# Kernel tuning notes

Measured on AMD Instinct MI355X. Metric: run time of the kernel, lower is better.

Reference implementation:

```python
import jax, jax.numpy as jnp
import numpy as np

B, D = 32768, 512
DEPTH = 7
ORDERS = (1, 2, 3, 5)
COUPLING_STRENGTH = 1.0


def _damping_coeffs():
    # frequency_dependent profile: 0.1 / (1 + exp(linspace(0, 3, D)))
    freqs = jnp.exp(jnp.linspace(0.0, 3.0, D))
    return 0.1 / (1.0 + freqs)


def _generate_harmonics(wave, hmats):
    acc = jnp.zeros_like(wave)
    for order, H in zip(ORDERS, hmats):
        hw = wave @ H.astype(wave.dtype)
        if order == 1:
            h = hw
        elif order == 2:
            h = hw * jnp.conj(hw)
        elif order == 3:
            h = hw * jnp.conj(hw) * hw
        else:
            mag = jnp.abs(hw)
            ph = jnp.angle(hw)
            h = (mag ** (1.0 / order)) * jnp.exp(1j * (ph * float(order)))
        acc = acc + h * (1.0 / (order * order))
    return acc


def _nonlinearity(wave, scale, bias):
    re = jnp.tanh(wave.real * scale + bias)
    im = jnp.tanh(wave.imag * scale + bias)
    return jax.lax.complex(re, im)


def _forward(wave_real, wave_imag, coupling_matrix, harmonic_1, harmonic_2,
             harmonic_3, harmonic_5, mixing_scale, mixing_bias):
    wave = jax.lax.complex(wave_real, wave_imag)  # [B, D] complex64
    hmats = (harmonic_1, harmonic_2, harmonic_3, harmonic_5)
    damping = _damping_coeffs()  # [D], non-trainable constant

    chamber = wave
    history = []
    for depth in range(DEPTH):
        transformed = (chamber @ coupling_matrix.astype(chamber.dtype)) * COUPLING_STRENGTH
        with_harmonics = transformed + _generate_harmonics(chamber, hmats)
        if depth > 0:
            # InterferenceLayer approximated as complex wave superposition
            interference = chamber + with_harmonics
        else:
            interference = with_harmonics
        nl = _nonlinearity(interference, mixing_scale, mixing_bias)
        factor = jnp.exp(-damping * float(depth)).astype(jnp.float32)
        chamber = nl * factor.astype(nl.dtype)
        history.append(chamber)

    w = jnp.exp(-jnp.linspace(0.0, 2.0, DEPTH))
    w = w / jnp.sum(w)
    stacked = jnp.stack(history)  # [DEPTH, B, D]
    out = jnp.sum(stacked * w[:, None, None].astype(stacked.dtype), axis=0)
    return out


def setup_inputs() -> dict:
    key = jax.random.key(0)
    ks = jax.random.split(key, 8)
    s = 1.0 / np.sqrt(D)  # approx orthogonal init scale
    return {
        "wave_real": jax.random.normal(ks[0], (B, D), jnp.float32),
        "wave_imag": jax.random.normal(ks[1], (B, D), jnp.float32),
        "coupling_matrix": jax.random.normal(ks[2], (D, D), jnp.float32) * s,
        "harmonic_1": jax.random.normal(ks[3], (D, D), jnp.float32) * s,
        "harmonic_2": jax.random.normal(ks[4], (D, D), jnp.float32) * s,
        "harmonic_3": jax.random.normal(ks[5], (D, D), jnp.float32) * s,
        "harmonic_5": jax.random.normal(ks[6], (D, D), jnp.float32) * s,
        "mixing_scale": jnp.ones((D,), jnp.float32),
        "mixing_bias": jnp.zeros((D,), jnp.float32),
    }


def reference(wave_real, wave_imag, coupling_matrix, harmonic_1, harmonic_2,
              harmonic_3, harmonic_5, mixing_scale, mixing_bias):
    out = _forward(wave_real, wave_imag, coupling_matrix, harmonic_1,
                   harmonic_2, harmonic_3, harmonic_5, mixing_scale, mixing_bias)
    # return as stacked real/imag float32 [2, B, D] for harness comparability
    return jnp.stack([out.real, out.imag])
```

## Files before the change

### kernel.cpp

```cpp
#include <hip/hip_runtime.h>
#include <hip/hip_bf16.h>
#include <cstdint>


typedef __bf16 bf16_t;
typedef bf16_t bf16x8 __attribute__((ext_vector_type(8)));
typedef float f32x4 __attribute__((ext_vector_type(4)));
typedef _Float16 h2_t __attribute__((ext_vector_type(2)));

#define B_ROWS 32768
#define D_DIM 512
#define N_DEPTH 7
#define BD ((size_t)B_ROWS * D_DIM)

__device__ __forceinline__ unsigned short f2b(float f) {
  bf16_t h = (bf16_t)f;
  return __builtin_bit_cast(unsigned short, h);
}
__device__ __forceinline__ float b2f(unsigned short u) {
  bf16_t h = __builtin_bit_cast(bf16_t, u);
  return (float)h;
}
__device__ __forceinline__ float fast_tanh(float x) {
  float ax = fabsf(x);
  float e = __expf(2.0f * ax);
  float t = 1.0f - 2.0f / (e + 1.0f);
  return copysignf(t, x);
}
__device__ __forceinline__ int lds_addr(int row, int byte_in_row) {
  return row * 1024 + (byte_in_row ^ ((row & 7) << 4));
}

__global__ __launch_bounds__(256) void prepack_v2(
    const float* __restrict__ cm, const float* __restrict__ h1,
    const float* __restrict__ h2, const float* __restrict__ h3,
    const float* __restrict__ h5, unsigned short* __restrict__ dst) {
  int gid = blockIdx.x * 256 + threadIdx.x;
  if (gid >= 32 * 16 * 64) return;
  int l  = gid & 63;
  int ks = (gid >> 6) & 15;
  int t  = gid >> 10;
  int n  = t * 16 + (l & 15);
  int k0 = ks * 32 + (l >> 4) * 8;
  unsigned short* base = dst + ((size_t)(t * 16 + ks) * 6) * 512 + l * 8;
  bf16x8 f0, f1, f2, f3, f4, f5;
#pragma unroll
  for (int i = 0; i < 8; ++i) {
    size_t idx = (size_t)(k0 + i) * D_DIM + n;
    float v0 = cm[idx] + h1[idx];
    unsigned short h0 = f2b(v0);
    f0[i] = __builtin_bit_cast(bf16_t, h0);
    f1[i] = (bf16_t)(v0 - b2f(h0));
    f2[i] = (bf16_t)h2[idx];
    f3[i] = (bf16_t)h3[idx];
    float v5 = h5[idx];
    unsigned short h5v = f2b(v5);
    f4[i] = __builtin_bit_cast(bf16_t, h5v);
    f5[i] = (bf16_t)(v5 - b2f(h5v));
  }
  *(bf16x8*)(base + 0 * 512) = f0;
  *(bf16x8*)(base + 1 * 512) = f1;
  *(bf16x8*)(base + 2 * 512) = f2;
  *(bf16x8*)(base + 3 * 512) = f3;
  *(bf16x8*)(base + 4 * 512) = f4;
  *(bf16x8*)(base + 5 * 512) = f5;
}

__global__ __launch_bounds__(1024) void resonance_kernel(
    const float* __restrict__ wr, const float* __restrict__ wi,
    const float* __restrict__ scale, const float* __restrict__ bias,
    const unsigned short* __restrict__ pre, float* __restrict__ out) {
  __shared__ unsigned short lds_hi[2][32 * 512];
  __shared__ unsigned short lds_lo[2][32 * 512];

  const int tid  = threadIdx.x;
  const int lane = tid & 63;
  const int wave = tid >> 6;
  const int ln15 = lane & 15;
  const int lg   = lane >> 4;
  const int r0   = blockIdx.x * 16;

#pragma unroll
  for (int it = 0; it < 2; ++it) {
    int idx = it * 1024 + tid;
    int row = idx >> 6;
    int k0  = (idx & 63) * 8;
    const float* src = (row < 16)
        ? (wr + (size_t)(r0 + row) * D_DIM + k0)
        : (wi + (size_t)(r0 + row - 16) * D_DIM + k0);
    float4 v0 = *(const float4*)(src);
    float4 v1 = *(const float4*)(src + 4);
    float v[8] = {v0.x, v0.y, v0.z, v0.w, v1.x, v1.y, v1.z, v1.w};
    bf16x8 ph, pl;
#pragma unroll
    for (int j = 0; j < 8; ++j) {
      unsigned short h = f2b(v[j]);
      ph[j] = __builtin_bit_cast(bf16_t, h);
      pl[j] = (bf16_t)(v[j] - b2f(h));
    }
    int ad = lds_addr(row, k0 * 2);
    *(bf16x8*)((char*)lds_hi[0] + ad) = ph;
    *(bf16x8*)((char*)lds_lo[0] + ad) = pl;
  }
  __syncthreads();

  float Wsum = 0.0f;
#pragma unroll
  for (int d = 0; d < N_DEPTH; ++d) Wsum += __expf(-(float)d * (1.0f / 3.0f));
  const float invW = 1.0f / Wsum;

  h2_t oacc[2][4];
#pragma unroll
  for (int c = 0; c < 2; ++c)
#pragma unroll
    for (int r = 0; r < 4; ++r) oacc[c][r] = (h2_t){(_Float16)0.f, (_Float16)0.f};

  int cur = 0;
  for (int depth = 0; depth < N_DEPTH; ++depth) {
    const float wd = __expf(-(float)depth * (1.0f / 3.0f)) * invW;
    const char* Ahi = (const char*)lds_hi[cur];
    const char* Alo = (const char*)lds_lo[cur];
    char* Nhi = (char*)lds_hi[cur ^ 1];
    char* Nlo = (char*)lds_lo[cur ^ 1];

#pragma unroll
    for (int c = 0; c < 2; ++c) {
      const int t = c * 16 + wave;
      f32x4 acc0[2], acc1[2], acc2[2], acc3[2];
#pragma unroll
      for (int mt = 0; mt < 2; ++mt) {
        acc0[mt] = (f32x4){0.f, 0.f, 0.f, 0.f};
        acc1[mt] = (f32x4){0.f, 0.f, 0.f, 0.f};
        acc2[mt] = (f32x4){0.f, 0.f, 0.f, 0.f};
        acc3[mt] = (f32x4){0.f, 0.f, 0.f, 0.f};
      }

      const unsigned short* bb = pre + ((size_t)(t * 16) * 6 + 3) * 512 + lane * 8;
#pragma unroll 2
      for (int ks = 0; ks < 16; ++ks) {
        bf16x8 ah[2], al[2];
#pragma unroll
        for (int mt = 0; mt < 2; ++mt) {
          int ad = lds_addr(mt * 16 + ln15, ks * 64 + lg * 16);
          ah[mt] = *(const bf16x8*)(Ahi + ad);
          al[mt] = *(const bf16x8*)(Alo + ad);
        }
        bf16x8 b0h = *(const bf16x8*)(bb - 1536);
        bf16x8 b0l = *(const bf16x8*)(bb - 1024);
        bf16x8 b1h = *(const bf16x8*)(bb - 512);
        bf16x8 b2h = *(const bf16x8*)(bb);
        bf16x8 b3h = *(const bf16x8*)(bb + 512);
        bf16x8 b3l = *(const bf16x8*)(bb + 1024);
        bb += 3072;
#pragma unroll
        for (int mt = 0; mt < 2; ++mt) {
          acc0[mt] = __builtin_amdgcn_mfma_f32_16x16x32_bf16(ah[mt], b0h, acc0[mt], 0, 0, 0);
          acc0[mt] = __builtin_amdgcn_mfma_f32_16x16x32_bf16(al[mt], b0h, acc0[mt], 0, 0, 0);
          acc0[mt] = __builtin_amdgcn_mfma_f32_16x16x32_bf16(ah[mt], b0l, acc0[mt], 0, 0, 0);
          acc1[mt] = __builtin_amdgcn_mfma_f32_16x16x32_bf16(ah[mt], b1h, acc1[mt], 0, 0, 0);
          acc2[mt] = __builtin_amdgcn_mfma_f32_16x16x32_bf16(ah[mt], b2h, acc2[mt], 0, 0, 0);
          acc3[mt] = __builtin_amdgcn_mfma_f32_16x16x32_bf16(ah[mt], b3h, acc3[mt], 0, 0, 0);
          acc3[mt] = __builtin_amdgcn_mfma_f32_16x16x32_bf16(al[mt], b3h, acc3[mt], 0, 0, 0);
          acc3[mt] = __builtin_amdgcn_mfma_f32_16x16x32_bf16(ah[mt], b3l, acc3[mt], 0, 0, 0);
        }
      }

      const int col = t * 16 + ln15;
      const float sclv = scale[col];
      const float biav = bias[col];
      const float damp = 0.1f / (1.0f + __expf(3.0f * (float)col * (1.0f / 511.0f)));
      const float fac  = __expf(-damp * (float)depth);
#pragma unroll
      for (int r = 0; r < 4; ++r) {
        const int brow = lg * 4 + r;
        float lr = acc0[0][r],  li = acc0[1][r];
        float re2 = acc1[0][r], im2 = acc1[1][r];
        float ar = 0.25f * (re2 * re2 + im2 * im2);
        float re3 = acc2[0][r], im3 = acc2[1][r];
        float m3 = re3 * re3 + im3 * im3;
        ar += 0.111111111f * m3 * re3;
        float ai = 0.111111111f * m3 * im3;
        float re5 = acc3[0][r], im5 = acc3[1][r];
        float m5 = re5 * re5 + im5 * im5;
        {
          float m5c = fmaxf(m5, 1e-36f);
          float inv = rsqrtf(m5c);
          float ur = re5 * inv, ui = im5 * inv;
          float u2r = ur * ur - ui * ui,     u2i = 2.0f * ur * ui;
          float u4r = u2r * u2r - u2i * u2i, u4i = 2.0f * u2r * u2i;
          float u5r = u4r * ur - u4i * ui,   u5i = u4r * ui + u4i * ur;
          float mag = __expf(0.1f * __logf(m5c));
          float msk = (m5 > 1e-36f) ? 0.04f : 0.0f;
          ar += msk * mag * u5r;
          ai += msk * mag * u5i;
        }
        float ir = lr + ar, ii = li + ai;
        const int colb = col * 2;
        const int ar_ = lds_addr(brow, colb);
        const int ai_ = lds_addr(brow + 16, colb);
        if (depth > 0) {
          ir += b2f(*(const unsigned short*)(Ahi + ar_))
              + b2f(*(const unsigned short*)(Alo + ar_));
          ii += b2f(*(const unsigned short*)(Ahi + ai_))
              + b2f(*(const unsigned short*)(Alo + ai_));
        }
        float cre = fast_tanh(ir * sclv + biav) * fac;
        float cim = fast_tanh(ii * sclv + biav) * fac;
        oacc[c][r] += (h2_t){(_Float16)(wd * cre), (_Float16)(wd * cim)};
        if (depth < N_DEPTH - 1) {
          unsigned short hr = f2b(cre);
          unsigned short hi = f2b(cim);
          *(unsigned short*)(Nhi + ar_) = hr;
          *(unsigned short*)(Nlo + ar_) = f2b(cre - b2f(hr));
          *(unsigned short*)(Nhi + ai_) = hi;
          *(unsigned short*)(Nlo + ai_) = f2b(cim - b2f(hi));
        }
      }
    }
    __syncthreads();
    cur ^= 1;
  }

#pragma unroll
  for (int c = 0; c < 2; ++c) {
    const int col = (c * 16 + wave) * 16 + ln15;
#pragma unroll
    for (int r = 0; r < 4; ++r) {
      int brow = lg * 4 + r;
      size_t base = (size_t)(r0 + brow) * D_DIM + col;
      out[base] = (float)oacc[c][r][0];
      out[BD + base] = (float)oacc[c][r][1];
    }
  }
}

extern "C" void kernel_launch(void* const* d_in, const int* in_sizes, int n_in,
                              void* d_out, int out_size, void* d_ws, size_t ws_size,
                              hipStream_t stream) {
  const float* wr = (const float*)d_in[0];
  const float* wi = (const float*)d_in[1];
  const float* cm = (const float*)d_in[2];
  const float* h1 = (const float*)d_in[3];
  const float* h2 = (const float*)d_in[4];
  const float* h3 = (const float*)d_in[5];
  const float* h5 = (const float*)d_in[6];
  const float* sc = (const float*)d_in[7];
  const float* bi = (const float*)d_in[8];
  unsigned short* pre = (unsigned short*)d_ws;
  float* out = (float*)d_out;

  hipLaunchKernelGGL(prepack_v2, dim3(128), dim3(256), 0, stream,
                     cm, h1, h2, h3, h5, pre);
  hipLaunchKernelGGL(resonance_kernel, dim3(B_ROWS / 16), dim3(1024), 0, stream,
                     wr, wi, sc, bi, pre, out);
}
```

Before: 1.946 ms.

## Switch complex GEMMs from 16x16x32 to 32x32x16 MFMA tiles

Replaces the 16x16x32 bf16 MFMA with 32x32x16 MFMA so each wave computes a 32-row (16 real + 16 imag) by 32-column tile in one accumulator per harmonic, and repacks the weight layout to match. Each wave now covers one 32-column slice instead of two 16-column slices, which halves the per-wave loop passes and the B-operand reuse overhead and lets scale/bias/damping be hoisted out of the depth loop. The epilogue row mapping changes to follow the 32x32 accumulator layout. The cost is larger accumulators (64 floats), which raises register pressure at 1024 threads per block.

```diff
diff --git a/kernel.cpp b/kernel.cpp
--- a/kernel.cpp
+++ b/kernel.cpp
@@ -5,7 +5,7 @@
 
 typedef __bf16 bf16_t;
 typedef bf16_t bf16x8 __attribute__((ext_vector_type(8)));
-typedef float f32x4 __attribute__((ext_vector_type(4)));
+typedef float f32x16 __attribute__((ext_vector_type(16)));
 typedef _Float16 h2_t __attribute__((ext_vector_type(2)));
 
 #define B_ROWS 32768
@@ -31,18 +31,18 @@
   return row * 1024 + (byte_in_row ^ ((row & 7) << 4));
 }
 
-__global__ __launch_bounds__(256) void prepack_v2(
+__global__ __launch_bounds__(256) void prepack_v3(
     const float* __restrict__ cm, const float* __restrict__ h1,
     const float* __restrict__ h2, const float* __restrict__ h3,
     const float* __restrict__ h5, unsigned short* __restrict__ dst) {
   int gid = blockIdx.x * 256 + threadIdx.x;
-  if (gid >= 32 * 16 * 64) return;
+  if (gid >= 16 * 32 * 64) return;
   int l  = gid & 63;
-  int ks = (gid >> 6) & 15;
-  int t  = gid >> 10;
-  int n  = t * 16 + (l & 15);
-  int k0 = ks * 32 + (l >> 4) * 8;
-  unsigned short* base = dst + ((size_t)(t * 16 + ks) * 6) * 512 + l * 8;
+  int ks = (gid >> 6) & 31;
+  int t  = gid >> 11;
+  int n  = t * 32 + (l & 31);
+  int k0 = ks * 16 + (l >> 5) * 8;
+  unsigned short* base = dst + ((size_t)(t * 32 + ks) * 6) * 512 + l * 8;
   bf16x8 f0, f1, f2, f3, f4, f5;
 #pragma unroll
   for (int i = 0; i < 8; ++i) {
@@ -76,8 +76,8 @@
   const int tid  = threadIdx.x;
   const int lane = tid & 63;
   const int wave = tid >> 6;
-  const int ln15 = lane & 15;
-  const int lg   = lane >> 4;
+  const int l31  = lane & 31;
+  const int hh   = lane >> 5;
   const int r0   = blockIdx.x * 16;
 
 #pragma unroll
@@ -109,112 +109,94 @@
   for (int d = 0; d < N_DEPTH; ++d) Wsum += __expf(-(float)d * (1.0f / 3.0f));
   const float invW = 1.0f / Wsum;
 
-  h2_t oacc[2][4];
-#pragma unroll
-  for (int c = 0; c < 2; ++c)
-#pragma unroll
-    for (int r = 0; r < 4; ++r) oacc[c][r] = (h2_t){(_Float16)0.f, (_Float16)0.f};
+  const int col = wave * 32 + l31;
+  const float sclv = scale[col];
+  const float biav = bias[col];
+  const float damp = 0.1f / (1.0f + __expf(3.0f * (float)col * (1.0f / 511.0f)));
+
+  h2_t oacc[8];
+#pragma unroll
+  for (int j = 0; j < 8; ++j) oacc[j] = (h2_t){(_Float16)0.f, (_Float16)0.f};
 
   int cur = 0;
   for (int depth = 0; depth < N_DEPTH; ++depth) {
     const float wd = __expf(-(float)depth * (1.0f / 3.0f)) * invW;
+    const float fac = __expf(-damp * (float)depth);
     const char* Ahi = (const char*)lds_hi[cur];
     const char* Alo = (const char*)lds_lo[cur];
     char* Nhi = (char*)lds_hi[cur ^ 1];
     char* Nlo = (char*)lds_lo[cur ^ 1];
 
-#pragma unroll
-    for (int c = 0; c < 2; ++c) {
-      const int t = c * 16 + wave;
-      f32x4 acc0[2], acc1[2], acc2[2], acc3[2];
-#pragma unroll
-      for (int mt = 0; mt < 2; ++mt) {
-        acc0[mt] = (f32x4){0.f, 0.f, 0.f, 0.f};
-        acc1[mt] = (f32x4){0.f, 0.f, 0.f, 0.f};
-        acc2[mt] = (f32x4){0.f, 0.f, 0.f, 0.f};
-        acc3[mt] = (f32x4){0.f, 0.f, 0.f, 0.f};
+    f32x16 a0 = (f32x16)(0.f), a1 = (f32x16)(0.f);
+    f32x16 a2 = (f32x16)(0.f), a3 = (f32x16)(0.f);
+
+    const unsigned short* bb = pre + ((size_t)(wave * 32) * 6 + 3) * 512 + lane * 8;
+#pragma unroll 2
+    for (int ks = 0; ks < 32; ++ks) {
+      int ad = lds_addr(l31, ks * 32 + hh * 16);
+      bf16x8 ah = *(const bf16x8*)(Ahi + ad);
+      bf16x8 al = *(const bf16x8*)(Alo + ad);
+      bf16x8 b0h = *(const bf16x8*)(bb - 1536);
+      bf16x8 b0l = *(const bf16x8*)(bb - 1024);
+      bf16x8 b1h = *(const bf16x8*)(bb - 512);
+      bf16x8 b2h = *(const bf16x8*)(bb);
+      bf16x8 b3h = *(const bf16x8*)(bb + 512);
+      bf16x8 b3l = *(const bf16x8*)(bb + 1024);
+      bb += 3072;
+      a0 = __builtin_amdgcn_mfma_f32_32x32x16_bf16(ah, b0h, a0, 0, 0, 0);
+      a0 = __builtin_amdgcn_mfma_f32_32x32x16_bf16(al, b0h, a0, 0, 0, 0);
+      a0 = __builtin_amdgcn_mfma_f32_32x32x16_bf16(ah, b0l, a0, 0, 0, 0);
+      a1 = __builtin_amdgcn_mfma_f32_32x32x16_bf16(ah, b1h, a1, 0, 0, 0);
+      a2 = __builtin_amdgcn_mfma_f32_32x32x16_bf16(ah, b2h, a2, 0, 0, 0);
+      a3 = __builtin_amdgcn_mfma_f32_32x32x16_bf16(ah, b3h, a3, 0, 0, 0);
+      a3 = __builtin_amdgcn_mfma_f32_32x32x16_bf16(al, b3h, a3, 0, 0, 0);
+      a3 = __builtin_amdgcn_mfma_f32_32x32x16_bf16(ah, b3l, a3, 0, 0, 0);
+    }
+
+#pragma unroll
+    for (int j = 0; j < 8; ++j) {
+      const int crow = (j & 3) + 8 * (j >> 2) + 4 * hh;
+      float lr = a0[j],  li = a0[j + 8];
+      float re2 = a1[j], im2 = a1[j + 8];
+      float ar = 0.25f * (re2 * re2 + im2 * im2);
+      float re3 = a2[j], im3 = a2[j + 8];
+      float m3 = re3 * re3 + im3 * im3;
+      ar += 0.111111111f * m3 * re3;
+      float ai = 0.111111111f * m3 * im3;
+      float re5 = a3[j], im5 = a3[j + 8];
+      float m5 = re5 * re5 + im5 * im5;
+      {
+        float m5c = fmaxf(m5, 1e-36f);
+        float inv = rsqrtf(m5c);
+        float ur = re5 * inv, ui = im5 * inv;
+        float u2r = ur * ur - ui * ui,     u2i = 2.0f * ur * ui;
+        float u4r = u2r * u2r - u2i * u2i, u4i = 2.0f * u2r * u2i;
+        float u5r = u4r * ur - u4i * ui,   u5i = u4r * ui + u4i * ur;
+        float mag = __expf(0.1f * __logf(m5c));
+        float msk = (m5 > 1e-36f) ? 0.04f : 0.0f;
+        ar += msk * mag * u5r;
+        ai += msk * mag * u5i;
       }
-
-      const unsigned short* bb = pre + ((size_t)(t * 16) * 6 + 3) * 512 + lane * 8;
-#pragma unroll 2
-      for (int ks = 0; ks < 16; ++ks) {
-        bf16x8 ah[2], al[2];
-#pragma unroll
-        for (int mt = 0; mt < 2; ++mt) {
-          int ad = lds_addr(mt * 16 + ln15, ks * 64 + lg * 16);
-          ah[mt] = *(const bf16x8*)(Ahi + ad);
-          al[mt] = *(const bf16x8*)(Alo + ad);
-        }
-        bf16x8 b0h = *(const bf16x8*)(bb - 1536);
-        bf16x8 b0l = *(const bf16x8*)(bb - 1024);
-        bf16x8 b1h = *(const bf16x8*)(bb - 512);
-        bf16x8 b2h = *(const bf16x8*)(bb);
-        bf16x8 b3h = *(const bf16x8*)(bb + 512);
-        bf16x8 b3l = *(const bf16x8*)(bb + 1024);
-        bb += 3072;
-#pragma unroll
-        for (int mt = 0; mt < 2; ++mt) {
-          acc0[mt] = __builtin_amdgcn_mfma_f32_16x16x32_bf16(ah[mt], b0h, acc0[mt], 0, 0, 0);
-          acc0[mt] = __builtin_amdgcn_mfma_f32_16x16x32_bf16(al[mt], b0h, acc0[mt], 0, 0, 0);
-          acc0[mt] = __builtin_amdgcn_mfma_f32_16x16x32_bf16(ah[mt], b0l, acc0[mt], 0, 0, 0);
-          acc1[mt] = __builtin_amdgcn_mfma_f32_16x16x32_bf16(ah[mt], b1h, acc1[mt], 0, 0, 0);
-          acc2[mt] = __builtin_amdgcn_mfma_f32_16x16x32_bf16(ah[mt], b2h, acc2[mt], 0, 0, 0);
-          acc3[mt] = __builtin_amdgcn_mfma_f32_16x16x32_bf16(ah[mt], b3h, acc3[mt], 0, 0, 0);
-          acc3[mt] = __builtin_amdgcn_mfma_f32_16x16x32_bf16(al[mt], b3h, acc3[mt], 0, 0, 0);
-          acc3[mt] = __builtin_amdgcn_mfma_f32_16x16x32_bf16(ah[mt], b3l, acc3[mt], 0, 0, 0);
-        }
+      float ir = lr + ar, ii = li + ai;
+      const int colb = col * 2;
+      const int ar_ = lds_addr(crow, colb);
+      const int ai_ = lds_addr(crow + 16, colb);
+      if (depth > 0) {
+        ir += b2f(*(const unsigned short*)(Ahi + ar_))
+            + b2f(*(const unsigned short*)(Alo + ar_));
+        ii += b2f(*(const unsigned short*)(Ahi + ai_))
+            + b2f(*(const unsigned short*)(Alo + ai_));
       }
-
-      const int col = t * 16 + ln15;
-      const float sclv = scale[col];
-      const float biav = bias[col];
-      const float damp = 0.1f / (1.0f + __expf(3.0f * (float)col * (1.0f / 511.0f)));
-      const float fac  = __expf(-damp * (float)depth);
-#pragma unroll
-      for (int r = 0; r < 4; ++r) {
-        const int brow = lg * 4 + r;
-        float lr = acc0[0][r],  li = acc0[1][r];
-        float re2 = acc1[0][r], im2 = acc1[1][r];
-        float ar = 0.25f * (re2 * re2 + im2 * im2);
-        float re3 = acc2[0][r], im3 = acc2[1][r];
-        float m3 = re3 * re3 + im3 * im3;
-        ar += 0.111111111f * m3 * re3;
-        float ai = 0.111111111f * m3 * im3;
-        float re5 = acc3[0][r], im5 = acc3[1][r];
-        float m5 = re5 * re5 + im5 * im5;
-        {
-          float m5c = fmaxf(m5, 1e-36f);
-          float inv = rsqrtf(m5c);
-          float ur = re5 * inv, ui = im5 * inv;
-          float u2r = ur * ur - ui * ui,     u2i = 2.0f * ur * ui;
-          float u4r = u2r * u2r - u2i * u2i, u4i = 2.0f * u2r * u2i;
-          float u5r = u4r * ur - u4i * ui,   u5i = u4r * ui + u4i * ur;
-          float mag = __expf(0.1f * __logf(m5c));
-          float msk = (m5 > 1e-36f) ? 0.04f : 0.0f;
-          ar += msk * mag * u5r;
-          ai += msk * mag * u5i;
-        }
-        float ir = lr + ar, ii = li + ai;
-        const int colb = col * 2;
-        const int ar_ = lds_addr(brow, colb);
-        const int ai_ = lds_addr(brow + 16, colb);
-        if (depth > 0) {
-          ir += b2f(*(const unsigned short*)(Ahi + ar_))
-              + b2f(*(const unsigned short*)(Alo + ar_));
-          ii += b2f(*(const unsigned short*)(Ahi + ai_))
-              + b2f(*(const unsigned short*)(Alo + ai_));
-        }
-        float cre = fast_tanh(ir * sclv + biav) * fac;
-        float cim = fast_tanh(ii * sclv + biav) * fac;
-        oacc[c][r] += (h2_t){(_Float16)(wd * cre), (_Float16)(wd * cim)};
-        if (depth < N_DEPTH - 1) {
-          unsigned short hr = f2b(cre);
-          unsigned short hi = f2b(cim);
-          *(unsigned short*)(Nhi + ar_) = hr;
-          *(unsigned short*)(Nlo + ar_) = f2b(cre - b2f(hr));
-          *(unsigned short*)(Nhi + ai_) = hi;
-          *(unsigned short*)(Nlo + ai_) = f2b(cim - b2f(hi));
-        }
+      float cre = fast_tanh(ir * sclv + biav) * fac;
+      float cim = fast_tanh(ii * sclv + biav) * fac;
+      oacc[j] += (h2_t){(_Float16)(wd * cre), (_Float16)(wd * cim)};
+      if (depth < N_DEPTH - 1) {
+        unsigned short hr = f2b(cre);
+        unsigned short hi = f2b(cim);
+        *(unsigned short*)(Nhi + ar_) = hr;
+        *(unsigned short*)(Nlo + ar_) = f2b(cre - b2f(hr));
+        *(unsigned short*)(Nhi + ai_) = hi;
+        *(unsigned short*)(Nlo + ai_) = f2b(cim - b2f(hi));
       }
     }
     __syncthreads();
@@ -222,15 +204,11 @@
   }
 
 #pragma unroll
-  for (int c = 0; c < 2; ++c) {
-    const int col = (c * 16 + wave) * 16 + ln15;
-#pragma unroll
-    for (int r = 0; r < 4; ++r) {
-      int brow = lg * 4 + r;
-      size_t base = (size_t)(r0 + brow) * D_DIM + col;
-      out[base] = (float)oacc[c][r][0];
-      out[BD + base] = (float)oacc[c][r][1];
-    }
+  for (int j = 0; j < 8; ++j) {
+    const int crow = (j & 3) + 8 * (j >> 2) + 4 * hh;
+    size_t base = (size_t)(r0 + crow) * D_DIM + col;
+    out[base] = (float)oacc[j][0];
+    out[BD + base] = (float)oacc[j][1];
   }
 }
 
@@ -249,7 +227,7 @@
   unsigned short* pre = (unsigned short*)d_ws;
   float* out = (float*)d_out;
 
-  hipLaunchKernelGGL(prepack_v2, dim3(128), dim3(256), 0, stream,
+  hipLaunchKernelGGL(prepack_v3, dim3(128), dim3(256), 0, stream,
                      cm, h1, h2, h3, h5, pre);
   hipLaunchKernelGGL(resonance_kernel, dim3(B_ROWS / 16), dim3(1024), 0, stream,
                      wr, wi, sc, bi, pre, out);
```

Result: slower. 2.189 ms (+12.5%).
